# Kernel tuning notes

Measured on AMD Instinct MI355X. Metric: run time of the kernel, lower is better.

## Reference

```python
import jax, jax.numpy as jnp
import numpy as np

D_MODEL = 256; N_HEADS = 8; N_LEVELS = 4; N_POINTS = 4; NUM_ITER = 2
SHAPES = [(92, 160), (46, 80), (23, 40), (12, 20)]  # 4-level FPN, Len_in = 19560
LEN_IN = sum(h * w for h, w in SHAPES)
N_BATCH = 2


def _offset_bias():
    # faithful to _reset_parameters grid init of sampling_offsets.bias
    thetas = jnp.arange(N_HEADS, dtype=jnp.float32) * (2.0 * np.pi / N_HEADS)
    grid = jnp.stack([jnp.cos(thetas), jnp.sin(thetas)], -1)
    grid = grid / jnp.max(jnp.abs(grid), axis=-1, keepdims=True)
    grid = jnp.tile(grid[:, None, None, :], (1, N_LEVELS, N_POINTS, 1))
    grid = grid * (jnp.arange(N_POINTS, dtype=jnp.float32) + 1.0)[None, None, :, None]
    return grid.reshape(-1)


def setup_inputs() -> dict:
    key = jax.random.key(0)
    ks = jax.random.split(key, 12)
    N, Lq, d = N_BATCH, LEN_IN, D_MODEL
    s = 0.02
    return {
        "query0": jax.random.normal(ks[0], (N, Lq, d), jnp.float32),
        "query1": jax.random.normal(ks[1], (N, Lq, d), jnp.float32),
        "reference_points": jax.random.uniform(ks[2], (N, Lq, N_LEVELS, 2), jnp.float32),
        "input_flatten0": jax.random.normal(ks[3], (N, LEN_IN, d), jnp.float32),
        "input_flatten1": jax.random.normal(ks[4], (N, LEN_IN, d), jnp.float32),
        "input_spatial_shapes": jnp.array(SHAPES, jnp.int32),
        "input_level_start_index": jnp.array(np.cumsum([0] + [h * w for h, w in SHAPES[:-1]]), jnp.int32),
        "W_so": s * jax.random.normal(ks[5], (d, N_HEADS * N_LEVELS * N_POINTS * 2), jnp.float32),
        "b_so": _offset_bias(),
        "W_aw": s * jax.random.normal(ks[6], (d, N_HEADS * N_LEVELS * N_POINTS), jnp.float32),
        "b_aw": jnp.zeros((N_HEADS * N_LEVELS * N_POINTS,), jnp.float32),
        "W_v": s * jax.random.normal(ks[7], (d, d), jnp.float32),
        "b_v": jnp.zeros((d,), jnp.float32),
        "W_o": s * jax.random.normal(ks[8], (d, d), jnp.float32),
        "b_o": jnp.zeros((d,), jnp.float32),
        "W_agg": s * jax.random.normal(ks[9], (d * NUM_ITER, d), jnp.float32),
        "b_agg": jnp.zeros((d,), jnp.float32),
    }


def _sample_level(v_l, loc_l, H, W):
    # v_l: (N, nH, H*W, D); loc_l: (N, Lq, nH, P, 2) in [0,1]
    # bilinear, align_corners=False, zero padding (matches grid_sample fallback / CUDA kernel)
    x = loc_l[..., 0] * W - 0.5
    y = loc_l[..., 1] * H - 0.5
    x0 = jnp.floor(x); y0 = jnp.floor(y)

    def gather(xi, yi):
        inb = ((xi >= 0) & (xi <= W - 1) & (yi >= 0) & (yi <= H - 1)).astype(v_l.dtype)
        idx = (jnp.clip(yi, 0, H - 1) * W + jnp.clip(xi, 0, W - 1)).astype(jnp.int32)
        idx_t = jnp.transpose(idx, (0, 2, 1, 3))  # (N, nH, Lq, P)
        g = jax.vmap(jax.vmap(lambda vt, it: vt[it]))(v_l, idx_t)  # (N, nH, Lq, P, D)
        return g * jnp.transpose(inb, (0, 2, 1, 3))[..., None]

    def wt(w):
        return jnp.transpose(w, (0, 2, 1, 3))[..., None]

    return (wt((y0 + 1 - y) * (x0 + 1 - x)) * gather(x0, y0)
            + wt((y0 + 1 - y) * (x - x0)) * gather(x0 + 1, y0)
            + wt((y - y0) * (x0 + 1 - x)) * gather(x0, y0 + 1)
            + wt((y - y0) * (x - x0)) * gather(x0 + 1, y0 + 1))  # (N, nH, Lq, P, D)


def _ms_deform_attn(value, loc, attn, shapes, starts):
    # value: (N, Len_in, nH, D); loc: (N, Lq, nH, L, P, 2); attn: (N, Lq, nH, L, P)
    v = jnp.transpose(value, (0, 2, 1, 3))  # (N, nH, Len_in, D)
    acc = None
    for lvl in range(N_LEVELS):
        H, W = int(shapes[lvl, 0]), int(shapes[lvl, 1])
        s = int(starts[lvl])
        out_l = _sample_level(v[:, :, s:s + H * W], loc[:, :, :, lvl], H, W)
        a = jnp.transpose(attn[:, :, :, lvl], (0, 2, 1, 3))  # (N, nH, Lq, P)
        term = jnp.einsum('nhqpd,nhqp->nhqd', out_l, a)
        acc = term if acc is None else acc + term
    N, nH, Lq, D = acc.shape
    return jnp.transpose(acc, (0, 2, 1, 3)).reshape(N, Lq, nH * D)


def reference(query0, query1, reference_points, input_flatten0, input_flatten1,
              input_spatial_shapes, input_level_start_index,
              W_so, b_so, W_aw, b_aw, W_v, b_v, W_o, b_o, W_agg, b_agg):
    shapes = np.asarray(input_spatial_shapes)
    starts = np.asarray(input_level_start_index)
    N, Lq, d = query0.shape
    nH, L, P = N_HEADS, N_LEVELS, N_POINTS
    queries = [query0, query1]
    flats = [input_flatten0, input_flatten1]
    values, offs, aws = [], [], []
    for q, f in zip(queries, flats):
        values.append((f @ W_v + b_v).reshape(N, -1, nH, d // nH))
        offs.append((q @ W_so + b_so).reshape(N, Lq, nH, L, P, 2))
        aws.append((q @ W_aw + b_aw).reshape(N, Lq, nH, L * P))
    # joint softmax over num_iter * n_levels * n_points (the one-shot trick)
    aw_all = jax.nn.softmax(jnp.concatenate(aws, axis=-1), axis=-1)
    # (L, 2) normalizer = (W, H)
    normalizer = jnp.stack([input_spatial_shapes[..., 1], input_spatial_shapes[..., 0]], -1).astype(query0.dtype)
    outs = []
    for i in range(NUM_ITER):
        aw_i = aw_all[..., i * L * P:(i + 1) * L * P].reshape(N, Lq, nH, L, P)
        loc = reference_points[:, :, None, :, None, :] + offs[i] / normalizer[None, None, None, :, None, :]
        o = _ms_deform_attn(values[i], loc, aw_i, shapes, starts)
        outs.append(o @ W_o + b_o)
    return jnp.concatenate(outs, axis=-1) @ W_agg + b_agg
```

## Files before the change

### kernel.cpp

```cpp
#include <hip/hip_runtime.h>
#include <math.h>

#define NBATCH 2
#define LQ     19560
#define LEN    19560
#define NQ     (NBATCH * LQ)
#define DMODEL 256
#define NHEADS 8
#define HDIM   32
#define NLEV   4
#define NPTS   4
#define LDQS   384

typedef __bf16 bf16x8 __attribute__((ext_vector_type(8)));
typedef float  f32x4  __attribute__((ext_vector_type(4)));
typedef float  f32x2  __attribute__((ext_vector_type(2)));

__device__ inline unsigned short f2bf(float f) {
    unsigned int u = __float_as_uint(f);
    u += 0x7FFFu + ((u >> 16) & 1u);
    return (unsigned short)(u >> 16);
}
__device__ inline f32x2 bfpair(unsigned int u) {
    f32x2 r;
    r.x = __uint_as_float(u << 16);
    r.y = __uint_as_float(u & 0xFFFF0000u);
    return r;
}

__global__ __launch_bounds__(256) void prep_all(
    const float* __restrict__ q0, const float* __restrict__ q1,
    const float* __restrict__ f0, const float* __restrict__ f1,
    const float* __restrict__ Wv, const float* __restrict__ Wso,
    const float* __restrict__ Waw, const float* __restrict__ bso,
    const float* __restrict__ baw,
    const float* __restrict__ Wo, const float* __restrict__ Wagg,
    const float* __restrict__ bo, const float* __restrict__ bagg,
    unsigned short* __restrict__ Qb0, unsigned short* __restrict__ Qb1,
    unsigned short* __restrict__ Fb0, unsigned short* __restrict__ Fb1,
    unsigned short* __restrict__ Wvt, unsigned short* __restrict__ Wsoawt,
    float* __restrict__ bsoaw,
    unsigned short* __restrict__ Wfcat, float* __restrict__ bfused)
{
    const int b = blockIdx.x;
    if (b < 19560) {
        const int tsel = b / 4890;
        const int x = b - tsel * 4890;
        const float* s = (tsel & 2) ? ((tsel & 1) ? f1 : f0) : ((tsel & 1) ? q1 : q0);
        unsigned short* d = (tsel & 2) ? ((tsel & 1) ? Fb1 : Fb0) : ((tsel & 1) ? Qb1 : Qb0);
        size_t i = ((size_t)x * 256 + threadIdx.x) * 8;
        float4 a = *(const float4*)(s + i);
        float4 c = *(const float4*)(s + i + 4);
        union { uint4 u; unsigned short h[8]; } t;
        t.h[0] = f2bf(a.x); t.h[1] = f2bf(a.y); t.h[2] = f2bf(a.z); t.h[3] = f2bf(a.w);
        t.h[4] = f2bf(c.x); t.h[5] = f2bf(c.y); t.h[6] = f2bf(c.z); t.h[7] = f2bf(c.w);
        if (tsel & 2) {
            *(uint4*)(d + i) = t.u;
        } else {
            size_t row = i >> 8; int c8 = (int)(i & 255);
            *(uint4*)(d + row * 768 + 512 + c8) = t.u;
        }
    } else if (b < 19560 + 640) {
        int o = (b - 19560) * 256 + threadIdx.x;
        if (o < 65536) {
            int n = o >> 8, k = o & 255;
            Wvt[o] = f2bf(Wv[(size_t)k * 256 + n]);
        } else {
            int p = o - 65536;
            int n = p >> 8, k = p & 255;
            float v = (n < 256) ? Wso[(size_t)k * 256 + n] : Waw[(size_t)k * 128 + (n - 256)];
            Wsoawt[p] = f2bf(v);
        }
        if (o < 384) bsoaw[o] = (o < 256) ? bso[o] : baw[o - 256];
    } else {
        int k = b - 20200;
        int n = threadIdx.x;
        float s0 = 0.f, s1 = 0.f;
        for (int j = 0; j < 256; j++) {
            float w = Wo[k * 256 + j];
            s0 += w * Wagg[j * 256 + n];
            s1 += w * Wagg[(256 + j) * 256 + n];
        }
        Wfcat[(size_t)n * 512 + k]       = f2bf(s0);
        Wfcat[(size_t)n * 512 + 256 + k] = f2bf(s1);
        if (k == 0) {
            float bb = bagg[n];
            for (int j = 0; j < 256; j++)
                bb += bo[j] * (Wagg[j * 256 + n] + Wagg[(256 + j) * 256 + n]);
            bfused[n] = bb;
        }
    }
}

__global__ __launch_bounds__(256) void gemm_mid(
    const unsigned short* __restrict__ Qa0, const unsigned short* __restrict__ Qa1,
    const unsigned short* __restrict__ Fb0, const unsigned short* __restrict__ Fb1,
    const unsigned short* __restrict__ Wsoawt, const unsigned short* __restrict__ Wvt,
    const float* __restrict__ bsoaw, const float* __restrict__ bv,
    float* __restrict__ QS0, float* __restrict__ QS1,
    unsigned short* __restrict__ V0, unsigned short* __restrict__ V1)
{
    __shared__ __align__(16) unsigned short As[128 * 64];
    __shared__ __align__(16) unsigned short Bs[128 * 64];

    const int z = blockIdx.z;
    const int isOff = (z < 2);
    const int zz = z & 1;
    const unsigned short* A = isOff ? (zz ? Qa1 : Qa0) : (zz ? Fb1 : Fb0);
    const unsigned short* Bt = isOff ? Wsoawt : Wvt;
    const float* bias = isOff ? bsoaw : bv;
    const int lda = isOff ? 768 : 256;

    const int tid  = threadIdx.x;
    const int w    = tid >> 6, lane = tid & 63;
    const int wm = w >> 1, wn = w & 1;
    const int m0 = blockIdx.y * 128, n0 = blockIdx.x * 128;
    const int lr = lane & 15, quad = lane >> 4;

    const int sr  = lane >> 3;
    const int scl = (lane & 7) ^ sr;
    const int colb = scl * 8;
    size_t arow[4], brow[4];
    #pragma unroll
    for (int j = 0; j < 4; j++) {
        int r = (w * 4 + j) * 8 + sr;
        int ra = m0 + r; if (ra > NQ - 1) ra = NQ - 1;
        arow[j] = (size_t)ra * lda;
        brow[j] = (size_t)(n0 + r) * 256;
    }

    const f32x4 zero = {0.f, 0.f, 0.f, 0.f};
    f32x4 acc[4][4];
    #pragma unroll
    for (int i = 0; i < 4; i++)
        #pragma unroll
        for (int j = 0; j < 4; j++) acc[i][j] = zero;

    for (int t = 0; t < 256; t += 64) {
        #pragma unroll
        for (int j = 0; j < 4; j++) {
            int lofs = __builtin_amdgcn_readfirstlane((w * 4 + j) * 1024);
            __builtin_amdgcn_global_load_lds(
                (const __attribute__((address_space(1))) void*)(A + arow[j] + t + colb),
                (__attribute__((address_space(3))) void*)((char*)As + lofs), 16, 0, 0);
            __builtin_amdgcn_global_load_lds(
                (const __attribute__((address_space(1))) void*)(Bt + brow[j] + t + colb),
                (__attribute__((address_space(3))) void*)((char*)Bs + lofs), 16, 0, 0);
        }
        __syncthreads();

        #pragma unroll
        for (int kk = 0; kk < 2; kk++) {
            bf16x8 af[4], bff[4];
            #pragma unroll
            for (int mi = 0; mi < 4; mi++) {
                int R = wm * 64 + mi * 16 + lr;
                int pc = ((kk * 4 + quad) ^ (lr & 7)) * 16;
                af[mi] = *(const bf16x8*)((const char*)As + R * 128 + pc);
            }
            #pragma unroll
            for (int ni = 0; ni < 4; ni++) {
                int R = wn * 64 + ni * 16 + lr;
                int pc = ((kk * 4 + quad) ^ (lr & 7)) * 16;
                bff[ni] = *(const bf16x8*)((const char*)Bs + R * 128 + pc);
            }
            #pragma unroll
            for (int mi = 0; mi < 4; mi++)
                #pragma unroll
                for (int ni = 0; ni < 4; ni++)
                    acc[mi][ni] = __builtin_amdgcn_mfma_f32_16x16x32_bf16(
                        af[mi], bff[ni], acc[mi][ni], 0, 0, 0);
        }
        __syncthreads();
    }

    float* Cf = isOff ? (zz ? QS1 : QS0) : nullptr;
    unsigned short* Cb = isOff ? nullptr : (zz ? V1 : V0);
    #pragma unroll
    for (int mi = 0; mi < 4; mi++) {
        #pragma unroll
        for (int reg = 0; reg < 4; reg++) {
            int row = m0 + wm * 64 + mi * 16 + quad * 4 + reg;
            if (row >= NQ) continue;
            #pragma unroll
            for (int ni = 0; ni < 4; ni++) {
                int col = n0 + wn * 64 + ni * 16 + lr;
                float v = acc[mi][ni][reg] + bias[col];
                if (isOff) {
                    Cf[(size_t)row * LDQS + col] = v;
                } else {
                    int n = row >= LQ ? 1 : 0;
                    int pos = row - n * LQ;
                    int h = col >> 5, d = col & 31;
                    Cb[((size_t)(n * NHEADS + h) * LEN + pos) * HDIM + d] = f2bf(v);
                }
            }
        }
    }
}

__global__ __launch_bounds__(256) void gemm_logits(
    const unsigned short* __restrict__ Qa0, const unsigned short* __restrict__ Qa1,
    const unsigned short* __restrict__ Bt,
    const float* __restrict__ bias,
    float* __restrict__ C0, float* __restrict__ C1)
{
    __shared__ __align__(16) unsigned short As[128 * 64];
    __shared__ __align__(16) unsigned short Bs[128 * 64];

    const int tid  = threadIdx.x;
    const int w    = tid >> 6, lane = tid & 63;
    const int wm = w >> 1, wn = w & 1;
    const int m0 = blockIdx.x * 128;
    const int lr = lane & 15, quad = lane >> 4;

    const int sr  = lane >> 3;
    const int scl = (lane & 7) ^ sr;
    const int colb = scl * 8;
    size_t arow[4], brow[4];
    #pragma unroll
    for (int j = 0; j < 4; j++) {
        int r = (w * 4 + j) * 8 + sr;
        int ra = m0 + r; if (ra > NQ - 1) ra = NQ - 1;
        arow[j] = (size_t)ra * 768;
        brow[j] = (size_t)(256 + r) * 256;
    }

    const f32x4 zero = {0.f, 0.f, 0.f, 0.f};
    f32x4 acc[2][4][4];
    #pragma unroll
    for (int zz = 0; zz < 2; zz++)
        #pragma unroll
        for (int i = 0; i < 4; i++)
            #pragma unroll
            for (int j = 0; j < 4; j++) acc[zz][i][j] = zero;

    #pragma unroll
    for (int z = 0; z < 2; z++) {
        const unsigned short* A = z ? Qa1 : Qa0;
        for (int t = 0; t < 256; t += 64) {
            #pragma unroll
            for (int j = 0; j < 4; j++) {
                int lofs = __builtin_amdgcn_readfirstlane((w * 4 + j) * 1024);
                __builtin_amdgcn_global_load_lds(
                    (const __attribute__((address_space(1))) void*)(A + arow[j] + t + colb),
                    (__attribute__((address_space(3))) void*)((char*)As + lofs), 16, 0, 0);
                __builtin_amdgcn_global_load_lds(
                    (const __attribute__((address_space(1))) void*)(Bt + brow[j] + t + colb),
                    (__attribute__((address_space(3))) void*)((char*)Bs + lofs), 16, 0, 0);
            }
            __syncthreads();
            #pragma unroll
            for (int kk = 0; kk < 2; kk++) {
                bf16x8 af[4], bff[4];
                #pragma unroll
                for (int mi = 0; mi < 4; mi++) {
                    int R = wm * 64 + mi * 16 + lr;
                    int pc = ((kk * 4 + quad) ^ (lr & 7)) * 16;
                    af[mi] = *(const bf16x8*)((const char*)As + R * 128 + pc);
                }
                #pragma unroll
                for (int ni = 0; ni < 4; ni++) {
                    int R = wn * 64 + ni * 16 + lr;
                    int pc = ((kk * 4 + quad) ^ (lr & 7)) * 16;
                    bff[ni] = *(const bf16x8*)((const char*)Bs + R * 128 + pc);
                }
                #pragma unroll
                for (int mi = 0; mi < 4; mi++)
                    #pragma unroll
                    for (int ni = 0; ni < 4; ni++)
                        acc[z][mi][ni] = __builtin_amdgcn_mfma_f32_16x16x32_bf16(
                            af[mi], bff[ni], acc[z][mi][ni], 0, 0, 0);
            }
            __syncthreads();
        }
    }

    float bv[4];
    #pragma unroll
    for (int ni = 0; ni < 4; ni++) bv[ni] = bias[256 + wn * 64 + ni * 16 + lr];

    #pragma unroll
    for (int mi = 0; mi < 4; mi++) {
        #pragma unroll
        for (int reg = 0; reg < 4; reg++) {
            int row = m0 + wm * 64 + mi * 16 + quad * 4 + reg;
            #pragma unroll
            for (int ni = 0; ni < 4; ni++) {
                float a = acc[0][mi][ni][reg] + bv[ni];
                float c = acc[1][mi][ni][reg] + bv[ni];
                float m = fmaxf(a, c);
                #pragma unroll
                for (int d = 1; d < 16; d <<= 1) m = fmaxf(m, __shfl_xor(m, d));
                float ea = expf(a - m), ec = expf(c - m);
                float s = ea + ec;
                #pragma unroll
                for (int d = 1; d < 16; d <<= 1) s += __shfl_xor(s, d);
                float inv = 1.0f / s;
                if (row < NQ) {
                    int col = 256 + wn * 64 + ni * 16 + lr;
                    C0[(size_t)row * LDQS + col] = ea * inv;
                    C1[(size_t)row * LDQS + col] = ec * inv;
                }
            }
        }
    }
}

#define QCHUNK 64
#define CHUNKS ((LQ + QCHUNK - 1) / QCHUNK)

__global__ __launch_bounds__(256) void ms_sample(
    const unsigned short* __restrict__ V0, const unsigned short* __restrict__ V1,
    const float* __restrict__ QS0, const float* __restrict__ QS1,
    const float* __restrict__ refp, unsigned short* __restrict__ Ocat)
{
    __shared__ unsigned short Sidx[16][65][4];
    __shared__ float          Swt [16][65][4];

    const int b = blockIdx.x;
    const int h = b & 7;
    const int rest = b >> 3;
    const int chunk = rest % CHUNKS;
    const int inn   = rest / CHUNKS;
    const int n  = inn & 1;
    const int it = inn >> 1;

    const int tid = threadIdx.x;
    const int ql  = tid >> 2;
    const int lj  = tid & 3;
    const int qraw = chunk * QCHUNK + ql;
    const bool valid = qraw < LQ;
    const int q  = valid ? qraw : LQ - 1;
    const int nq = n * LQ + q;

    const unsigned short* __restrict__ val = it ? V1 : V0;
    const float* __restrict__ QS = it ? QS1 : QS0;
    const unsigned short* __restrict__ vb2 =
        val + (size_t)(n * NHEADS + h) * LEN * HDIM;

    const int Hs[4] = {92, 46, 23, 12};
    const int Ws[4] = {160, 80, 40, 20};
    const int Ss[4] = {0, 14720, 18400, 19320};

    const float* prow = QS + (size_t)nq * LDQS;

    {
        const int H = Hs[lj], W = Ws[lj], S = Ss[lj];
        const float4 o0 = *(const float4*)(prow + (h << 5) + lj * 8);
        const float4 o1 = *(const float4*)(prow + (h << 5) + lj * 8 + 4);
        const float4 a4 = *(const float4*)(prow + 256 + (h << 4) + lj * 4);
        const float2 rp = *(const float2*)(refp + (size_t)nq * 8 + lj * 2);
        const float fx = rp.x * (float)W - 0.5f;
        const float fy = rp.y * (float)H - 0.5f;
        const float oxs[4] = {o0.x, o0.z, o1.x, o1.z};
        const float oys[4] = {o0.y, o0.w, o1.y, o1.w};
        const float avs[4] = {a4.x, a4.y, a4.z, a4.w};
        #pragma unroll
        for (int k = 0; k < NPTS; k++) {
            const float x = fx + oxs[k];
            const float y = fy + oys[k];
            const float x0f = floorf(x), y0f = floorf(y);
            const int x0 = (int)x0f, y0 = (int)y0f;
            const float wx1 = x - x0f, wy1 = y - y0f;
            const float wx0 = 1.0f - wx1, wy0 = 1.0f - wy1;
            const int xc0 = min(max(x0, 0), W - 1);
            const int xc1 = min(max(x0 + 1, 0), W - 1);
            const int yc0 = min(max(y0, 0), H - 1);
            const int yc1 = min(max(y0 + 1, 0), H - 1);
            const float a = avs[k];
            const float ay0 = ((unsigned int)y0 < (unsigned int)H) ? a * wy0 : 0.f;
            const float ay1 = ((unsigned int)(y0 + 1) < (unsigned int)H) ? a * wy1 : 0.f;
            const float mx0 = ((unsigned int)x0 < (unsigned int)W) ? wx0 : 0.f;
            const float mx1 = ((unsigned int)(x0 + 1) < (unsigned int)W) ? wx1 : 0.f;
            const int r0 = S + yc0 * W, r1 = S + yc1 * W;
            union { uint2 u; unsigned short s4[4]; } ip;
            ip.s4[0] = (unsigned short)(r0 + xc0);
            ip.s4[1] = (unsigned short)(r0 + xc1);
            ip.s4[2] = (unsigned short)(r1 + xc0);
            ip.s4[3] = (unsigned short)(r1 + xc1);
            *(uint2*)&Sidx[lj * 4 + k][ql][0] = ip.u;
            float4 w4 = make_float4(ay0 * mx0, ay0 * mx1, ay1 * mx0, ay1 * mx1);
            *(float4*)&Swt[lj * 4 + k][ql][0] = w4;
        }
    }
    __syncthreads();

    const int dl = lj << 3;
    const unsigned short* __restrict__ vdl = vb2 + dl;

    f32x2 acc[4];
    #pragma unroll
    for (int i = 0; i < 4; i++) acc[i] = (f32x2){0.f, 0.f};

    auto corner = [&](unsigned int eo, float wgt) {
        const uint4 c = *(const uint4*)(vdl + eo);
        const f32x2 w2 = {wgt, wgt};
        acc[0] += w2 * bfpair(c.x);
        acc[1] += w2 * bfpair(c.y);
        acc[2] += w2 * bfpair(c.z);
        acc[3] += w2 * bfpair(c.w);
    };

    #pragma unroll
    for (int p = 0; p < 16; p++) {
        const uint2 i2 = *(const uint2*)&Sidx[p][ql][0];
        const float4 w4 = *(const float4*)&Swt[p][ql][0];
        corner((i2.x & 0xFFFFu) << 5, w4.x);
        corner((i2.x >> 16) << 5, w4.y);
        corner((i2.y & 0xFFFFu) << 5, w4.z);
        corner((i2.y >> 16) << 5, w4.w);
    }

    if (valid) {
        union { uint4 u; unsigned short s[8]; } t;
        #pragma unroll
        for (int i = 0; i < 4; i++) {
            t.s[2 * i]     = f2bf(acc[i].x);
            t.s[2 * i + 1] = f2bf(acc[i].y);
        }
        *(uint4*)&Ocat[(size_t)nq * 512 + it * 256 + h * HDIM + dl] = t.u;
    }
}

__global__ __launch_bounds__(256) void gemm_tail(
    const unsigned short* __restrict__ A, const unsigned short* __restrict__ Bt,
    const float* __restrict__ bias, float* __restrict__ C)
{
    __shared__ __align__(16) unsigned short As[128 * 64];
    __shared__ __align__(16) unsigned short Bs[128 * 64];

    const int tid  = threadIdx.x;
    const int w    = tid >> 6, lane = tid & 63;
    const int wm = w >> 1, wn = w & 1;
    const int m0 = blockIdx.y * 128, n0 = blockIdx.x * 128;
    const int lr = lane & 15, quad = lane >> 4;

    const int sr  = lane >> 3;
    const int scl = (lane & 7) ^ sr;
    const int colb = scl * 8;
    size_t arow[4], brow[4];
    #pragma unroll
    for (int j = 0; j < 4; j++) {
        int r = (w * 4 + j) * 8 + sr;
        int ra = m0 + r; if (ra > NQ - 1) ra = NQ - 1;
        arow[j] = (size_t)ra * 512;
        brow[j] = (size_t)(n0 + r) * 512;
    }

    const f32x4 zero = {0.f, 0.f, 0.f, 0.f};
    f32x4 acc[4][4];
    #pragma unroll
    for (int i = 0; i < 4; i++)
        #pragma unroll
        for (int j = 0; j < 4; j++) acc[i][j] = zero;

    for (int t = 0; t < 512; t += 64) {
        #pragma unroll
        for (int j = 0; j < 4; j++) {
            int lofs = __builtin_amdgcn_readfirstlane((w * 4 + j) * 1024);
            __builtin_amdgcn_global_load_lds(
                (const __attribute__((address_space(1))) void*)(A + arow[j] + t + colb),
                (__attribute__((address_space(3))) void*)((char*)As + lofs), 16, 0, 0);
            __builtin_amdgcn_global_load_lds(
                (const __attribute__((address_space(1))) void*)(Bt + brow[j] + t + colb),
                (__attribute__((address_space(3))) void*)((char*)Bs + lofs), 16, 0, 0);
        }
        __syncthreads();

        #pragma unroll
        for (int kk = 0; kk < 2; kk++) {
            bf16x8 af[4], bff[4];
            #pragma unroll
            for (int mi = 0; mi < 4; mi++) {
                int R = wm * 64 + mi * 16 + lr;
                int pc = ((kk * 4 + quad) ^ (lr & 7)) * 16;
                af[mi] = *(const bf16x8*)((const char*)As + R * 128 + pc);
            }
            #pragma unroll
            for (int ni = 0; ni < 4; ni++) {
                int R = wn * 64 + ni * 16 + lr;
                int pc = ((kk * 4 + quad) ^ (lr & 7)) * 16;
                bff[ni] = *(const bf16x8*)((const char*)Bs + R * 128 + pc);
            }
            #pragma unroll
            for (int mi = 0; mi < 4; mi++)
                #pragma unroll
                for (int ni = 0; ni < 4; ni++)
                    acc[mi][ni] = __builtin_amdgcn_mfma_f32_16x16x32_bf16(
                        af[mi], bff[ni], acc[mi][ni], 0, 0, 0);
        }
        __syncthreads();
    }

    #pragma unroll
    for (int mi = 0; mi < 4; mi++) {
        #pragma unroll
        for (int reg = 0; reg < 4; reg++) {
            int row = m0 + wm * 64 + mi * 16 + quad * 4 + reg;
            if (row >= NQ) continue;
            #pragma unroll
            for (int ni = 0; ni < 4; ni++) {
                int col = n0 + wn * 64 + ni * 16 + lr;
                C[(size_t)row * 256 + col] = acc[mi][ni][reg] + bias[col];
            }
        }
    }
}

extern "C" void kernel_launch(void* const* d_in, const int* in_sizes, int n_in,
                              void* d_out, int out_size, void* d_ws, size_t ws_size,
                              hipStream_t stream)
{
    const float* q0    = (const float*)d_in[0];
    const float* q1    = (const float*)d_in[1];
    const float* refp  = (const float*)d_in[2];
    const float* f0    = (const float*)d_in[3];
    const float* f1    = (const float*)d_in[4];
    const float* W_so  = (const float*)d_in[7];
    const float* b_so  = (const float*)d_in[8];
    const float* W_aw  = (const float*)d_in[9];
    const float* b_aw  = (const float*)d_in[10];
    const float* W_v   = (const float*)d_in[11];
    const float* b_v   = (const float*)d_in[12];
    const float* W_o   = (const float*)d_in[13];
    const float* b_o   = (const float*)d_in[14];
    const float* W_agg = (const float*)d_in[15];
    const float* b_agg = (const float*)d_in[16];
    float* out = (float*)d_out;

    float* ws = (float*)d_ws;
    float* QS0 = ws;
    float* QS1 = QS0 + (size_t)NQ * LDQS;
    unsigned short* V0   = (unsigned short*)(QS1 + (size_t)NQ * LDQS);
    unsigned short* V1   = V0 + (size_t)NQ * 256;
    unsigned short* Ocat = V1 + (size_t)NQ * 256;
    unsigned short* Wvt    = Ocat + (size_t)NQ * 512;
    unsigned short* Wsoawt = Wvt + 65536;
    unsigned short* Wfcat  = Wsoawt + 98304;
    float* bsoaw = (float*)(Wfcat + 131072);
    float* bfus  = bsoaw + 384;

    unsigned short* Qb0 = (unsigned short*)QS0;
    unsigned short* Qb1 = (unsigned short*)QS1;
    unsigned short* Fb0 = Ocat;
    unsigned short* Fb1 = Ocat + (size_t)NQ * 256;
    const unsigned short* Qa0 = (const unsigned short*)QS0 + 512;
    const unsigned short* Qa1 = (const unsigned short*)QS1 + 512;

    const int MB = (NQ + 127) / 128;
    dim3 blk(256);

    prep_all<<<20456, blk, 0, stream>>>(
        q0, q1, f0, f1, W_v, W_so, W_aw, b_so, b_aw, W_o, W_agg, b_o, b_agg,
        Qb0, Qb1, Fb0, Fb1, Wvt, Wsoawt, bsoaw, Wfcat, bfus);

    gemm_mid<<<dim3(2, MB, 4), blk, 0, stream>>>(
        Qa0, Qa1, Fb0, Fb1, Wsoawt, Wvt, bsoaw, b_v, QS0, QS1, V0, V1);

    gemm_logits<<<MB, blk, 0, stream>>>(Qa0, Qa1, Wsoawt, bsoaw, QS0, QS1);

    ms_sample<<<2 * 2 * CHUNKS * 8, blk, 0, stream>>>(V0, V1, QS0, QS1, refp, Ocat);

    gemm_tail<<<dim3(2, MB, 1), blk, 0, stream>>>(Ocat, Wfcat, bfus, out);
}
```

Baseline: 480.0 us.

## Fold logits GEMM into mid GEMM and move joint softmax into sampler

The separate logits GEMM kernel is removed. Raw attention logits are now computed as extra z-slices of the mid GEMM, written to a separate workspace buffer when one is available. The joint softmax over both iterations moves into ms_sample, which reads both logit sets and reduces across lanes with shuffles. The sampler also stores 32-bit pre-shifted corner offsets in shared memory instead of packed 16-bit indices, which doubles that LDS footprint but drops the unpack work in the inner loop. The change saves a launch and a pass over the logits, at the cost of computing the softmax twice (once per iteration) and extra logit reads in the sampler.

```diff
diff --git a/kernel.cpp b/kernel.cpp
--- a/kernel.cpp
+++ b/kernel.cpp
@@ -92,24 +92,30 @@
     }
 }
 
-__global__ __launch_bounds__(256) void gemm_mid(
+__global__ __launch_bounds__(256) void gemm_mega(
     const unsigned short* __restrict__ Qa0, const unsigned short* __restrict__ Qa1,
     const unsigned short* __restrict__ Fb0, const unsigned short* __restrict__ Fb1,
     const unsigned short* __restrict__ Wsoawt, const unsigned short* __restrict__ Wvt,
     const float* __restrict__ bsoaw, const float* __restrict__ bv,
     float* __restrict__ QS0, float* __restrict__ QS1,
-    unsigned short* __restrict__ V0, unsigned short* __restrict__ V1)
+    unsigned short* __restrict__ V0, unsigned short* __restrict__ V1,
+    float* __restrict__ AW0, float* __restrict__ AW1, int awld, int zbase)
 {
+    const int z = blockIdx.z + zbase;
+    const int isVal = (z >= 2 && z < 4);
+    const int isLog = (z >= 4);
+    if (isLog && blockIdx.x != 0) return;
+    const int zz = z & 1;
+
     __shared__ __align__(16) unsigned short As[128 * 64];
     __shared__ __align__(16) unsigned short Bs[128 * 64];
 
-    const int z = blockIdx.z;
-    const int isOff = (z < 2);
-    const int zz = z & 1;
-    const unsigned short* A = isOff ? (zz ? Qa1 : Qa0) : (zz ? Fb1 : Fb0);
-    const unsigned short* Bt = isOff ? Wsoawt : Wvt;
-    const float* bias = isOff ? bsoaw : bv;
-    const int lda = isOff ? 768 : 256;
+    const unsigned short* A = isVal ? (zz ? Fb1 : Fb0) : (zz ? Qa1 : Qa0);
+    const unsigned short* Bt = isVal ? Wvt : Wsoawt;
+    const float* bias = isVal ? bv : bsoaw;
+    const int lda = isVal ? 256 : 768;
+    const int btrow0 = isLog ? 256 : 0;
+    const int bias0 = btrow0;
 
     const int tid  = threadIdx.x;
     const int w    = tid >> 6, lane = tid & 63;
@@ -126,7 +132,7 @@
         int r = (w * 4 + j) * 8 + sr;
         int ra = m0 + r; if (ra > NQ - 1) ra = NQ - 1;
         arow[j] = (size_t)ra * lda;
-        brow[j] = (size_t)(n0 + r) * 256;
+        brow[j] = (size_t)(btrow0 + n0 + r) * 256;
     }
 
     const f32x4 zero = {0.f, 0.f, 0.f, 0.f};
@@ -174,8 +180,9 @@
         __syncthreads();
     }
 
-    float* Cf = isOff ? (zz ? QS1 : QS0) : nullptr;
-    unsigned short* Cb = isOff ? nullptr : (zz ? V1 : V0);
+    float* Cf = isLog ? (zz ? AW1 : AW0) : (zz ? QS1 : QS0);
+    const int ldc = isLog ? awld : LDQS;
+    unsigned short* Cb = zz ? V1 : V0;
     #pragma unroll
     for (int mi = 0; mi < 4; mi++) {
         #pragma unroll
@@ -185,9 +192,9 @@
             #pragma unroll
             for (int ni = 0; ni < 4; ni++) {
                 int col = n0 + wn * 64 + ni * 16 + lr;
-                float v = acc[mi][ni][reg] + bias[col];
-                if (isOff) {
-                    Cf[(size_t)row * LDQS + col] = v;
+                float v = acc[mi][ni][reg] + bias[bias0 + col];
+                if (!isVal) {
+                    Cf[(size_t)row * ldc + col] = v;
                 } else {
                     int n = row >= LQ ? 1 : 0;
                     int pos = row - n * LQ;
@@ -199,124 +206,17 @@
     }
 }
 
-__global__ __launch_bounds__(256) void gemm_logits(
-    const unsigned short* __restrict__ Qa0, const unsigned short* __restrict__ Qa1,
-    const unsigned short* __restrict__ Bt,
-    const float* __restrict__ bias,
-    float* __restrict__ C0, float* __restrict__ C1)
-{
-    __shared__ __align__(16) unsigned short As[128 * 64];
-    __shared__ __align__(16) unsigned short Bs[128 * 64];
-
-    const int tid  = threadIdx.x;
-    const int w    = tid >> 6, lane = tid & 63;
-    const int wm = w >> 1, wn = w & 1;
-    const int m0 = blockIdx.x * 128;
-    const int lr = lane & 15, quad = lane >> 4;
-
-    const int sr  = lane >> 3;
-    const int scl = (lane & 7) ^ sr;
-    const int colb = scl * 8;
-    size_t arow[4], brow[4];
-    #pragma unroll
-    for (int j = 0; j < 4; j++) {
-        int r = (w * 4 + j) * 8 + sr;
-        int ra = m0 + r; if (ra > NQ - 1) ra = NQ - 1;
-        arow[j] = (size_t)ra * 768;
-        brow[j] = (size_t)(256 + r) * 256;
-    }
-
-    const f32x4 zero = {0.f, 0.f, 0.f, 0.f};
-    f32x4 acc[2][4][4];
-    #pragma unroll
-    for (int zz = 0; zz < 2; zz++)
-        #pragma unroll
-        for (int i = 0; i < 4; i++)
-            #pragma unroll
-            for (int j = 0; j < 4; j++) acc[zz][i][j] = zero;
-
-    #pragma unroll
-    for (int z = 0; z < 2; z++) {
-        const unsigned short* A = z ? Qa1 : Qa0;
-        for (int t = 0; t < 256; t += 64) {
-            #pragma unroll
-            for (int j = 0; j < 4; j++) {
-                int lofs = __builtin_amdgcn_readfirstlane((w * 4 + j) * 1024);
-                __builtin_amdgcn_global_load_lds(
-                    (const __attribute__((address_space(1))) void*)(A + arow[j] + t + colb),
-                    (__attribute__((address_space(3))) void*)((char*)As + lofs), 16, 0, 0);
-                __builtin_amdgcn_global_load_lds(
-                    (const __attribute__((address_space(1))) void*)(Bt + brow[j] + t + colb),
-                    (__attribute__((address_space(3))) void*)((char*)Bs + lofs), 16, 0, 0);
-            }
-            __syncthreads();
-            #pragma unroll
-            for (int kk = 0; kk < 2; kk++) {
-                bf16x8 af[4], bff[4];
-                #pragma unroll
-                for (int mi = 0; mi < 4; mi++) {
-                    int R = wm * 64 + mi * 16 + lr;
-                    int pc = ((kk * 4 + quad) ^ (lr & 7)) * 16;
-                    af[mi] = *(const bf16x8*)((const char*)As + R * 128 + pc);
-                }
-                #pragma unroll
-                for (int ni = 0; ni < 4; ni++) {
-                    int R = wn * 64 + ni * 16 + lr;
-                    int pc = ((kk * 4 + quad) ^ (lr & 7)) * 16;
-                    bff[ni] = *(const bf16x8*)((const char*)Bs + R * 128 + pc);
-                }
-                #pragma unroll
-                for (int mi = 0; mi < 4; mi++)
-                    #pragma unroll
-                    for (int ni = 0; ni < 4; ni++)
-                        acc[z][mi][ni] = __builtin_amdgcn_mfma_f32_16x16x32_bf16(
-                            af[mi], bff[ni], acc[z][mi][ni], 0, 0, 0);
-            }
-            __syncthreads();
-        }
-    }
-
-    float bv[4];
-    #pragma unroll
-    for (int ni = 0; ni < 4; ni++) bv[ni] = bias[256 + wn * 64 + ni * 16 + lr];
-
-    #pragma unroll
-    for (int mi = 0; mi < 4; mi++) {
-        #pragma unroll
-        for (int reg = 0; reg < 4; reg++) {
-            int row = m0 + wm * 64 + mi * 16 + quad * 4 + reg;
-            #pragma unroll
-            for (int ni = 0; ni < 4; ni++) {
-                float a = acc[0][mi][ni][reg] + bv[ni];
-                float c = acc[1][mi][ni][reg] + bv[ni];
-                float m = fmaxf(a, c);
-                #pragma unroll
-                for (int d = 1; d < 16; d <<= 1) m = fmaxf(m, __shfl_xor(m, d));
-                float ea = expf(a - m), ec = expf(c - m);
-                float s = ea + ec;
-                #pragma unroll
-                for (int d = 1; d < 16; d <<= 1) s += __shfl_xor(s, d);
-                float inv = 1.0f / s;
-                if (row < NQ) {
-                    int col = 256 + wn * 64 + ni * 16 + lr;
-                    C0[(size_t)row * LDQS + col] = ea * inv;
-                    C1[(size_t)row * LDQS + col] = ec * inv;
-                }
-            }
-        }
-    }
-}
-
 #define QCHUNK 64
 #define CHUNKS ((LQ + QCHUNK - 1) / QCHUNK)
 
 __global__ __launch_bounds__(256) void ms_sample(
     const unsigned short* __restrict__ V0, const unsigned short* __restrict__ V1,
     const float* __restrict__ QS0, const float* __restrict__ QS1,
+    const float* __restrict__ AW0, const float* __restrict__ AW1, int awld,
     const float* __restrict__ refp, unsigned short* __restrict__ Ocat)
 {
-    __shared__ unsigned short Sidx[16][65][4];
-    __shared__ float          Swt [16][65][4];
+    __shared__ unsigned int Sidx[16][65][4];
+    __shared__ float        Swt [16][65][4];
 
     const int b = blockIdx.x;
     const int h = b & 7;
@@ -346,16 +246,32 @@
     const float* prow = QS + (size_t)nq * LDQS;
 
     {
+        const float4 l0 = *(const float4*)(AW0 + (size_t)nq * awld + (h << 4) + lj * 4);
+        const float4 l1 = *(const float4*)(AW1 + (size_t)nq * awld + (h << 4) + lj * 4);
+        float m = fmaxf(fmaxf(fmaxf(l0.x, l0.y), fmaxf(l0.z, l0.w)),
+                        fmaxf(fmaxf(l1.x, l1.y), fmaxf(l1.z, l1.w)));
+        m = fmaxf(m, __shfl_xor(m, 1));
+        m = fmaxf(m, __shfl_xor(m, 2));
+        float e0x = expf(l0.x - m), e0y = expf(l0.y - m);
+        float e0z = expf(l0.z - m), e0w = expf(l0.w - m);
+        float e1x = expf(l1.x - m), e1y = expf(l1.y - m);
+        float e1z = expf(l1.z - m), e1w = expf(l1.w - m);
+        float s = ((e0x + e0y) + (e0z + e0w)) + ((e1x + e1y) + (e1z + e1w));
+        s += __shfl_xor(s, 1);
+        s += __shfl_xor(s, 2);
+        const float inv = 1.0f / s;
+        float avs[4];
+        if (it) { avs[0] = e1x * inv; avs[1] = e1y * inv; avs[2] = e1z * inv; avs[3] = e1w * inv; }
+        else    { avs[0] = e0x * inv; avs[1] = e0y * inv; avs[2] = e0z * inv; avs[3] = e0w * inv; }
+
         const int H = Hs[lj], W = Ws[lj], S = Ss[lj];
         const float4 o0 = *(const float4*)(prow + (h << 5) + lj * 8);
         const float4 o1 = *(const float4*)(prow + (h << 5) + lj * 8 + 4);
-        const float4 a4 = *(const float4*)(prow + 256 + (h << 4) + lj * 4);
         const float2 rp = *(const float2*)(refp + (size_t)nq * 8 + lj * 2);
         const float fx = rp.x * (float)W - 0.5f;
         const float fy = rp.y * (float)H - 0.5f;
         const float oxs[4] = {o0.x, o0.z, o1.x, o1.z};
         const float oys[4] = {o0.y, o0.w, o1.y, o1.w};
-        const float avs[4] = {a4.x, a4.y, a4.z, a4.w};
         #pragma unroll
         for (int k = 0; k < NPTS; k++) {
             const float x = fx + oxs[k];
@@ -374,12 +290,12 @@
             const float mx0 = ((unsigned int)x0 < (unsigned int)W) ? wx0 : 0.f;
             const float mx1 = ((unsigned int)(x0 + 1) < (unsigned int)W) ? wx1 : 0.f;
             const int r0 = S + yc0 * W, r1 = S + yc1 * W;
-            union { uint2 u; unsigned short s4[4]; } ip;
-            ip.s4[0] = (unsigned short)(r0 + xc0);
-            ip.s4[1] = (unsigned short)(r0 + xc1);
-            ip.s4[2] = (unsigned short)(r1 + xc0);
-            ip.s4[3] = (unsigned short)(r1 + xc1);
-            *(uint2*)&Sidx[lj * 4 + k][ql][0] = ip.u;
+            uint4 eo4;
+            eo4.x = (unsigned int)(r0 + xc0) << 5;
+            eo4.y = (unsigned int)(r0 + xc1) << 5;
+            eo4.z = (unsigned int)(r1 + xc0) << 5;
+            eo4.w = (unsigned int)(r1 + xc1) << 5;
+            *(uint4*)&Sidx[lj * 4 + k][ql][0] = eo4;
             float4 w4 = make_float4(ay0 * mx0, ay0 * mx1, ay1 * mx0, ay1 * mx1);
             *(float4*)&Swt[lj * 4 + k][ql][0] = w4;
         }
@@ -404,12 +320,12 @@
 
     #pragma unroll
     for (int p = 0; p < 16; p++) {
-        const uint2 i2 = *(const uint2*)&Sidx[p][ql][0];
+        const uint4 i4 = *(const uint4*)&Sidx[p][ql][0];
         const float4 w4 = *(const float4*)&Swt[p][ql][0];
-        corner((i2.x & 0xFFFFu) << 5, w4.x);
-        corner((i2.x >> 16) << 5, w4.y);
-        corner((i2.y & 0xFFFFu) << 5, w4.z);
-        corner((i2.y >> 16) << 5, w4.w);
+        corner(i4.x, w4.x);
+        corner(i4.y, w4.y);
+        corner(i4.z, w4.z);
+        corner(i4.w, w4.w);
     }
 
     if (valid) {
@@ -540,6 +456,7 @@
     unsigned short* Wfcat  = Wsoawt + 98304;
     float* bsoaw = (float*)(Wfcat + 131072);
     float* bfus  = bsoaw + 384;
+    float* wsend = bfus + 256;
 
     unsigned short* Qb0 = (unsigned short*)QS0;
     unsigned short* Qb1 = (unsigned short*)QS1;
@@ -548,6 +465,21 @@
     const unsigned short* Qa0 = (const unsigned short*)QS0 + 512;
     const unsigned short* Qa1 = (const unsigned short*)QS1 + 512;
 
+    size_t aw_bytes = (size_t)NQ * 128 * 4 * 2;
+    size_t need_merged = ((size_t)((char*)wsend - (char*)ws)) + aw_bytes;
+    const int merged = ws_size >= need_merged;
+    float *AW0, *AW1;
+    int awld;
+    if (merged) {
+        AW0 = wsend;
+        AW1 = AW0 + (size_t)NQ * 128;
+        awld = 128;
+    } else {
+        AW0 = QS0 + 256;
+        AW1 = QS1 + 256;
+        awld = LDQS;
+    }
+
     const int MB = (NQ + 127) / 128;
     dim3 blk(256);
 
@@ -555,12 +487,21 @@
         q0, q1, f0, f1, W_v, W_so, W_aw, b_so, b_aw, W_o, W_agg, b_o, b_agg,
         Qb0, Qb1, Fb0, Fb1, Wvt, Wsoawt, bsoaw, Wfcat, bfus);
 
-    gemm_mid<<<dim3(2, MB, 4), blk, 0, stream>>>(
-        Qa0, Qa1, Fb0, Fb1, Wsoawt, Wvt, bsoaw, b_v, QS0, QS1, V0, V1);
-
-    gemm_logits<<<MB, blk, 0, stream>>>(Qa0, Qa1, Wsoawt, bsoaw, QS0, QS1);
-
-    ms_sample<<<2 * 2 * CHUNKS * 8, blk, 0, stream>>>(V0, V1, QS0, QS1, refp, Ocat);
+    if (merged) {
+        gemm_mega<<<dim3(2, MB, 6), blk, 0, stream>>>(
+            Qa0, Qa1, Fb0, Fb1, Wsoawt, Wvt, bsoaw, b_v,
+            QS0, QS1, V0, V1, AW0, AW1, awld, 0);
+    } else {
+        gemm_mega<<<dim3(2, MB, 4), blk, 0, stream>>>(
+            Qa0, Qa1, Fb0, Fb1, Wsoawt, Wvt, bsoaw, b_v,
+            QS0, QS1, V0, V1, AW0, AW1, awld, 0);
+        gemm_mega<<<dim3(1, MB, 2), blk, 0, stream>>>(
+            Qa0, Qa1, Fb0, Fb1, Wsoawt, Wvt, bsoaw, b_v,
+            QS0, QS1, V0, V1, AW0, AW1, awld, 4);
+    }
+
+    ms_sample<<<2 * 2 * CHUNKS * 8, blk, 0, stream>>>(
+        V0, V1, QS0, QS1, AW0, AW1, awld, refp, Ocat);
 
     gemm_tail<<<dim3(2, MB, 1), blk, 0, stream>>>(Ocat, Wfcat, bfus, out);
 }
```

Result: no change. 474.2 us (-1.2%).
